# Kernel tuning notes

Measured on AMD Instinct MI355X. Metric: run time of the kernel, lower is better.

Reference implementation:

```python
import jax, jax.numpy as jnp
from jax import lax
import numpy as np

WS = 8        # window size
SHIFT = 4     # shift size
HEADS = 4
EPS = 1e-5


def _rel_pos_index(ws):
    coords = np.stack(np.meshgrid(np.arange(ws), np.arange(ws), indexing='ij'))  # (2,ws,ws)
    cf = coords.reshape(2, -1)
    rel = cf[:, :, None] - cf[:, None, :]           # (2,n,n)
    rel = rel.transpose(1, 2, 0).astype(np.int64)   # (n,n,2)
    rel[:, :, 0] += ws - 1
    rel[:, :, 1] += ws - 1
    rel[:, :, 0] *= 2 * ws - 1
    return rel.sum(-1)                              # (n,n)


def _attn_mask(h, w, ws, ss):
    img = np.zeros((h, w), dtype=np.float32)
    cnt = 0
    for hs in (slice(0, -ws), slice(-ws, -ss), slice(-ss, None)):
        for wsl in (slice(0, -ws), slice(-ws, -ss), slice(-ss, None)):
            img[hs, wsl] = cnt
            cnt += 1
    mw = img.reshape(h // ws, ws, w // ws, ws).transpose(0, 2, 1, 3).reshape(-1, ws * ws)
    am = mw[:, None, :] - mw[:, :, None]            # (nW,n,n)
    return np.where(am != 0, -100.0, 0.0).astype(np.float32)


def _ln(x, w, b):
    mu = x.mean(-1, keepdims=True)
    var = jnp.var(x, axis=-1, keepdims=True)
    return (x - mu) * lax.rsqrt(var + EPS) * w + b


def setup_inputs() -> dict:
    key = jax.random.key(0)
    ks = jax.random.split(key, 16)
    b, c, h, w = 4, 64, 256, 256
    hidden = 4 * c
    n_bias = (2 * WS - 1) * (2 * WS - 1)
    s = 0.02
    return {
        'x': jax.random.normal(ks[0], (b, c, h, w), jnp.float32),
        'norm1_w': jnp.ones((c,), jnp.float32),
        'norm1_b': jnp.zeros((c,), jnp.float32),
        'qkv_w': jax.random.normal(ks[1], (3 * c, c), jnp.float32) * s,
        'qkv_b': jnp.zeros((3 * c,), jnp.float32),
        'rpb': jax.random.normal(ks[2], (n_bias, HEADS), jnp.float32) * s,
        'proj_w': jax.random.normal(ks[3], (c, c), jnp.float32) * s,
        'proj_b': jnp.zeros((c,), jnp.float32),
        'norm2_w': jnp.ones((c,), jnp.float32),
        'norm2_b': jnp.zeros((c,), jnp.float32),
        'fc1_w': jax.random.normal(ks[4], (hidden, c), jnp.float32) * s,
        'fc1_b': jnp.zeros((hidden,), jnp.float32),
        'dw_w': jax.random.normal(ks[5], (hidden, 1, 5, 5), jnp.float32) * s,
        'dw_b': jnp.zeros((hidden,), jnp.float32),
        'fc2_w': jax.random.normal(ks[6], (c, hidden), jnp.float32) * s,
        'fc2_b': jnp.zeros((c,), jnp.float32),
    }


def reference(x, norm1_w, norm1_b, qkv_w, qkv_b, rpb, proj_w, proj_b,
              norm2_w, norm2_b, fc1_w, fc1_b, dw_w, dw_b, fc2_w, fc2_b):
    b, c, h, w = x.shape
    d = c // HEADS
    scale = d ** (-0.5)
    n = WS * WS

    x3 = jnp.transpose(x.reshape(b, c, h * w), (0, 2, 1))  # (b, hw, c)
    shortcut = x3
    xn = _ln(x3, norm1_w, norm1_b).reshape(b, h, w, c)

    # cyclic shift + window partition
    sx = jnp.roll(xn, (-SHIFT, -SHIFT), axis=(1, 2))
    win = sx.reshape(b, h // WS, WS, w // WS, WS, c).transpose(0, 1, 3, 2, 4, 5).reshape(-1, n, c)
    B_ = win.shape[0]

    qkv = (win @ qkv_w.T + qkv_b).reshape(B_, n, 3, HEADS, d).transpose(2, 0, 3, 1, 4)
    q, k, v = qkv[0] * scale, qkv[1], qkv[2]   # (B_, H, n, d)
    attn = jnp.einsum('bhnd,bhmd->bhnm', q, k)  # (B_, H, n, n)

    bias = rpb[jnp.asarray(_rel_pos_index(WS)).reshape(-1)].reshape(n, n, HEADS).transpose(2, 0, 1)
    attn = attn + bias[None]

    mask = jnp.asarray(_attn_mask(h, w, WS, SHIFT))  # (nW, n, n)
    nW = mask.shape[0]
    attn = attn.reshape(B_ // nW, nW, HEADS, n, n) + mask[None, :, None]
    attn = jax.nn.softmax(attn.reshape(B_, HEADS, n, n), axis=-1)

    out = jnp.einsum('bhnm,bhmd->bhnd', attn, v).transpose(0, 2, 1, 3).reshape(B_, n, c)
    out = out @ proj_w.T + proj_b

    # window reverse + un-shift
    sx = out.reshape(b, h // WS, w // WS, WS, WS, c).transpose(0, 1, 3, 2, 4, 5).reshape(b, h, w, c)
    xr = jnp.roll(sx, (SHIFT, SHIFT), axis=(1, 2)).reshape(b, h * w, c)
    x3 = shortcut + xr

    # ConvFFN
    xn = _ln(x3, norm2_w, norm2_b)
    hid = jax.nn.gelu(xn @ fc1_w.T + fc1_b, approximate=False)  # (b, hw, hidden)
    hidden = hid.shape[-1]
    himg = hid.transpose(0, 2, 1).reshape(b, hidden, h, w)
    dc = lax.conv_general_dilated(himg, dw_w, (1, 1), [(2, 2), (2, 2)],
                                  dimension_numbers=('NCHW', 'OIHW', 'NCHW'),
                                  feature_group_count=hidden)
    dc = jax.nn.gelu(dc + dw_b[None, :, None, None], approximate=False)
    hid = hid + dc.reshape(b, hidden, h * w).transpose(0, 2, 1)
    x3 = x3 + (hid @ fc2_w.T + fc2_b)

    return jnp.transpose(x3, (0, 2, 1)).reshape(b, c, h, w)
```

## Files before the change

kernel.cpp:

```cpp
#include <hip/hip_runtime.h>
#include <hip/hip_bf16.h>
#include <hip/hip_fp8.h>
#include <math.h>


typedef __bf16  bf16x8  __attribute__((ext_vector_type(8)));
typedef float   f32x4   __attribute__((ext_vector_type(4)));
typedef float   f32x2   __attribute__((ext_vector_type(2)));
typedef unsigned short ushortx8 __attribute__((ext_vector_type(8)));

__device__ __forceinline__ float gelu_f(float v) {
    float u = v * fmaf(0.0713548354f, v * v, 1.5957691216f);
    float t = __expf(u);
    float r = __builtin_amdgcn_rcpf(t + 1.0f);
    return v - v * r;
}
__device__ __forceinline__ unsigned char f32_to_fp8(float v) {
    __hip_fp8_e4m3 t(v);
    return (unsigned char)t.__x;
}
__device__ __forceinline__ float fp8_to_f32(unsigned char u) {
    __hip_fp8_e4m3 t;
    t.__x = (__hip_fp8_storage_t)u;
    return (float)t;
}

#if __has_builtin(__builtin_amdgcn_cvt_pk_f32_fp8) && __has_builtin(__builtin_amdgcn_cvt_pk_fp8_f32)
#define HW_FP8 1
#endif
template<bool HI>
__device__ __forceinline__ f32x2 fp8x2_f32(unsigned int u) {
#ifdef HW_FP8
    return __builtin_amdgcn_cvt_pk_f32_fp8((int)u, HI);
#else
    f32x2 r;
    const int s = HI ? 16 : 0;
    r.x = fp8_to_f32((unsigned char)(u >> s));
    r.y = fp8_to_f32((unsigned char)(u >> (s + 8)));
    return r;
#endif
}
template<bool HI>
__device__ __forceinline__ unsigned int f32x2_fp8(float a, float b, unsigned int old) {
#ifdef HW_FP8
    return (unsigned int)__builtin_amdgcn_cvt_pk_fp8_f32(a, b, (int)old, HI);
#else
    unsigned int v = (unsigned int)f32_to_fp8(a) | ((unsigned int)f32_to_fp8(b) << 8);
    return HI ? ((old & 0x0000ffffu) | (v << 16)) : ((old & 0xffff0000u) | v);
#endif
}

__device__ __forceinline__ unsigned short f2bf(float f) {
    unsigned int u = __builtin_bit_cast(unsigned int, f);
    u += 0x7fffu + ((u >> 16) & 1u);
    return (unsigned short)(u >> 16);
}
__device__ __forceinline__ float bf2f(unsigned short u) {
    return __builtin_bit_cast(float, ((unsigned int)u) << 16);
}

__global__ __launch_bounds__(256) void k_prep(
        const float* __restrict__ qkvw, const float* __restrict__ projw,
        const float* __restrict__ rpb,  const float* __restrict__ fc1w,
        unsigned short* __restrict__ qkvw_bf, unsigned short* __restrict__ projw_bf,
        unsigned short* __restrict__ rpb_bf,  unsigned short* __restrict__ fc1w_bf) {
    const int i = blockIdx.x * 256 + threadIdx.x;
    if (i < 12288) qkvw_bf[i] = f2bf(qkvw[i]);
    if (i < 4096)  projw_bf[i] = f2bf(projw[i]);
    if (i < 900)   rpb_bf[i]   = f2bf(rpb[i]);
    if (i < 16384) fc1w_bf[i]  = f2bf(fc1w[i]);
}

__global__ __launch_bounds__(256) void k_cvt(const float* __restrict__ src,
        unsigned short* __restrict__ dst, int n) {
    const int i = blockIdx.x * 256 + threadIdx.x;
    if (i < n) dst[i] = f2bf(src[i]);
}

__global__ __launch_bounds__(256) void k_ln1(const float* __restrict__ x,
        const float* __restrict__ w1, const float* __restrict__ b1,
        unsigned short* __restrict__ A, unsigned short* __restrict__ Bw) {
    __shared__ float tile[64 * 65];
    __shared__ float red0[256], red1[256];
    __shared__ float muv[64], rsv[64], lw[64], lb[64];
    const int tid = threadIdx.x;
    const int gid = blockIdx.x;
    const int xc = gid & 3, y = (gid >> 2) & 255, b = gid >> 10;
    const int x0 = xc * 64;
    if (tid < 64) { lw[tid] = w1[tid]; lb[tid] = b1[tid]; }

    const float* xb = x + ((size_t)b * 64) * 65536 + y * 256 + x0;
    {
        const int tk = tid & 63, cl = tid >> 6;
        for (int it = 0; it < 16; ++it) {
            int cc = cl + 4 * it;
            tile[cc * 65 + tk] = xb[(size_t)cc * 65536 + tk];
        }
    }
    __syncthreads();
    {
        const int tk = tid & 63, cl = tid >> 6;
        float s = 0.f, s2 = 0.f;
        #pragma unroll
        for (int k = 0; k < 16; ++k) {
            float v = tile[(cl * 16 + k) * 65 + tk];
            s += v; s2 += v * v;
        }
        red0[cl * 64 + tk] = s; red1[cl * 64 + tk] = s2;
    }
    __syncthreads();
    if (tid < 64) {
        float s  = red0[tid] + red0[64 + tid] + red0[128 + tid] + red0[192 + tid];
        float s2 = red1[tid] + red1[64 + tid] + red1[128 + tid] + red1[192 + tid];
        float mu = s * (1.f / 64.f);
        float var = s2 * (1.f / 64.f) - mu * mu;
        muv[tid] = mu; rsv[tid] = rsqrtf(var + 1e-5f);
    }
    __syncthreads();
    const int ch = tid & 63, tl = tid >> 6;
    const int ys = (y + 252) & 255;
    const int wy = ys >> 3, py = ys & 7;
    for (int it = 0; it < 16; ++it) {
        int t = tl + 4 * it;
        float v = tile[ch * 65 + t];
        int tok = (b << 16) + y * 256 + x0 + t;
        A[(size_t)tok * 64 + ch] = f2bf(v);
        float vn = (v - muv[t]) * rsv[t] * lw[ch] + lb[ch];
        int xs = (x0 + t + 252) & 255;
        int wx = xs >> 3, px = xs & 7;
        int widx = (b << 10) + (wy << 5) + wx;
        int pos = (py << 3) + px;
        Bw[((size_t)widx * 64 + pos) * 64 + ch] = f2bf(vn);
    }
}

__global__ __launch_bounds__(256) void k_attn(
        const unsigned short* __restrict__ Bw,
        const unsigned short* __restrict__ qkvw_bf,
        const unsigned short* __restrict__ projw_bf,
        const unsigned short* __restrict__ rpb_bf,
        const float* __restrict__ qkvb,
        const float* __restrict__ projb,
        const unsigned short* __restrict__ A, unsigned short* __restrict__ Cb) {
    __shared__ __align__(16) unsigned short Xs[4608];
    __shared__ __align__(16) unsigned short Ws[13824];
    __shared__ __align__(8)  unsigned short rpbl[900];
    __shared__ float qkvbl[192];
    __shared__ float projbl[64];

    const int tid = threadIdx.x;
    const int lane = tid & 63, wv = tid >> 6;
    const int l15 = lane & 15, quad = lane >> 4;
    const int widx = blockIdx.x;
    const int wib = widx & 1023;
    const int wy = wib >> 5, wx = wib & 31, bimg = widx >> 10;
    const bool edge = (wy == 31) | (wx == 31);

    const f32x4 zz = {0.f, 0.f, 0.f, 0.f};
    const ushortx8 zu = {0, 0, 0, 0, 0, 0, 0, 0};
    const bf16x8 z8 = __builtin_bit_cast(bf16x8, zu);

    const ushortx8 pw0 = *(const ushortx8*)(projw_bf + tid * 8);
    const ushortx8 pw1 = *(const ushortx8*)(projw_bf + (256 + tid) * 8);

    {
        const unsigned short* Xg = Bw + (size_t)widx * 4096 + wv * 1024;
        #pragma unroll
        for (int it = 0; it < 2; ++it) {
            int g = it * 64 + lane;
            int row = g >> 3, c8 = g & 7;
            *(ushortx8*)&Xs[(wv * 16 + row) * 72 + c8 * 8] =
                *(const ushortx8*)(Xg + g * 8);
        }
    }
    #pragma unroll
    for (int it = 0; it < 6; ++it) {
        int g = it * 256 + tid;
        int row = g >> 3, c8 = g & 7;
        *(ushortx8*)&Ws[row * 72 + c8 * 8] = *(const ushortx8*)(qkvw_bf + g * 8);
    }
    if (tid < 225) *(uint2*)&rpbl[tid * 4] = *(const uint2*)(rpb_bf + tid * 4);
    if (tid < 192) qkvbl[tid] = qkvb[tid];
    if (tid < 64)  projbl[tid] = projb[tid];
    __syncthreads();

    f32x4 qacc[12];
    #pragma unroll
    for (int i = 0; i < 12; ++i) qacc[i] = zz;
    {
        const bf16x8 av0 = *(const bf16x8*)&Xs[(16 * wv + l15) * 72 + quad * 8];
        const bf16x8 av1 = *(const bf16x8*)&Xs[(16 * wv + l15) * 72 + 32 + quad * 8];
        #pragma unroll
        for (int gl = 0; gl < 12; ++gl) {
            bf16x8 bv0 = *(const bf16x8*)&Ws[(gl * 16 + l15) * 72 + quad * 8];
            qacc[gl] = __builtin_amdgcn_mfma_f32_16x16x32_bf16(av0, bv0, qacc[gl], 0, 0, 0);
            bf16x8 bv1 = *(const bf16x8*)&Ws[(gl * 16 + l15) * 72 + 32 + quad * 8];
            qacc[gl] = __builtin_amdgcn_mfma_f32_16x16x32_bf16(av1, bv1, qacc[gl], 0, 0, 0);
        }
    }
    __syncthreads();

    #pragma unroll
    for (int g = 0; g < 12; ++g) {
        #pragma unroll
        for (int r = 0; r < 4; ++r) {
            int tok = 16 * wv + quad * 4 + r;
            int oc  = g * 16 + l15;
            float v = qacc[g][r] + qkvbl[oc];
            if (g < 4)       Ws[g * 1024 + tok * 16 + l15] = f2bf(v * 0.25f);
            else if (g < 8)  Ws[4096 + (g - 4) * 1024 + tok * 16 + l15] = f2bf(v);
            else             Ws[8192 + ((g - 8) * 16 + l15) * 72 + tok] = f2bf(v);
        }
    }
    __syncthreads();

    f32x4 sacc[4][4];
    #pragma unroll
    for (int h = 0; h < 4; ++h) {
        bf16x8 qa = z8;
        if (quad < 2) qa = *(const bf16x8*)&Ws[h * 1024 + (16 * wv + l15) * 16 + quad * 8];
        #pragma unroll
        for (int nt = 0; nt < 4; ++nt) {
            bf16x8 kf = z8;
            if (quad < 2) kf = *(const bf16x8*)&Ws[4096 + h * 1024 + (nt * 16 + l15) * 16 + quad * 8];
            sacc[h][nt] = __builtin_amdgcn_mfma_f32_16x16x32_bf16(qa, kf, zz, 0, 0, 0);
        }
    }
    __syncthreads();

    {
        const int r0 = tid >> 3;
        *(ushortx8*)&Ws[4096 + r0 * 64 + (((tid & 7) ^ (r0 & 7)) << 3)] = pw0;
        const int g1 = 256 + tid, r1 = g1 >> 3;
        *(ushortx8*)&Ws[4096 + r1 * 64 + (((g1 & 7) ^ (r1 & 7)) << 3)] = pw1;
    }

    const int jhi = l15 >> 3, jlo = l15 & 7;
    int offj4[4], regj[4];
    #pragma unroll
    for (int nt = 0; nt < 4; ++nt) {
        int j = nt * 16 + l15;
        int jy = j >> 3, jx = j & 7;
        offj4[nt] = (jy * 15 + jx) * 4;
        regj[nt] = 0;
        if (edge) {
            int ysj = wy * 8 + jy, xsj = wx * 8 + jx;
            regj[nt] = (ysj >= 252 ? 2 : (ysj >= 248 ? 1 : 0)) * 3
                     + (xsj >= 252 ? 2 : (xsj >= 248 ? 1 : 0));
        }
    }
    int rbA[4], regiA[4], pbaseA[4], i7A[4];
    #pragma unroll
    for (int r = 0; r < 4; ++r) {
        const int i = 16 * wv + quad * 4 + r;
        const int iy = i >> 3, ix = i & 7;
        rbA[r] = ((iy + 7) * 15 + (ix + 7)) * 4;
        i7A[r] = i & 7;
        pbaseA[r] = i * 64 + jlo;
        regiA[r] = 0;
        if (edge) {
            const int ysi = wy * 8 + iy, xsi = wx * 8 + ix;
            regiA[r] = (ysi >= 252 ? 2 : (ysi >= 248 ? 1 : 0)) * 3
                     + (xsi >= 252 ? 2 : (xsi >= 248 ? 1 : 0));
        }
    }

    f32x4 o[4];
    #pragma unroll
    for (int h = 0; h < 4; ++h) {
        float invh[4];
        #pragma unroll
        for (int r = 0; r < 4; ++r) {
            float m0 = -1e30f;
            #pragma unroll
            for (int nt = 0; nt < 4; ++nt) {
                float s = sacc[h][nt][r] + bf2f(rpbl[rbA[r] + h - offj4[nt]]);
                if (edge) s += (regj[nt] == regiA[r]) ? 0.f : -100.f;
                sacc[h][nt][r] = s;
                m0 = fmaxf(m0, s);
            }
            m0 = fmaxf(m0, __shfl_xor(m0, 1));
            m0 = fmaxf(m0, __shfl_xor(m0, 2));
            m0 = fmaxf(m0, __shfl_xor(m0, 4));
            m0 = fmaxf(m0, __shfl_xor(m0, 8));
            float s0 = 0.f;
            #pragma unroll
            for (int nt = 0; nt < 4; ++nt) {
                float e = __expf(sacc[h][nt][r] - m0);
                s0 += e;
                Ws[pbaseA[r] + ((((nt << 1) | jhi) ^ i7A[r]) << 3)] = f2bf(e);
            }
            s0 += __shfl_xor(s0, 1); s0 += __shfl_xor(s0, 2);
            s0 += __shfl_xor(s0, 4); s0 += __shfl_xor(s0, 8);
            invh[r] = 1.f / s0;
        }
        o[h] = zz;
        #pragma unroll
        for (int s = 0; s < 2; ++s) {
            bf16x8 pa = *(const bf16x8*)&Ws[(16 * wv + l15) * 64
                                            + (((s * 4 + quad) ^ (l15 & 7)) << 3)];
            bf16x8 vb = *(const bf16x8*)&Ws[8192 + (h * 16 + l15) * 72 + s * 32 + quad * 8];
            o[h] = __builtin_amdgcn_mfma_f32_16x16x32_bf16(pa, vb, o[h], 0, 0, 0);
        }
        #pragma unroll
        for (int r = 0; r < 4; ++r) o[h][r] *= invh[r];
    }

    unsigned short resid[16];
    #pragma unroll
    for (int r = 0; r < 4; ++r) {
        int tok = 16 * wv + quad * 4 + r;
        int py = tok >> 3, px = tok & 7;
        int yo = (wy * 8 + py + 4) & 255, xo = (wx * 8 + px + 4) & 255;
        size_t gt = ((size_t)bimg << 16) + yo * 256 + xo;
        #pragma unroll
        for (int nt = 0; nt < 4; ++nt)
            resid[r * 4 + nt] = A[gt * 64 + nt * 16 + l15];
    }

    #pragma unroll
    for (int h = 0; h < 4; ++h)
        #pragma unroll
        for (int r = 0; r < 4; ++r)
            Xs[(16 * wv + quad * 4 + r) * 72 + h * 16 + l15] = f2bf(o[h][r]);
    __syncthreads();

    f32x4 pacc[4];
    #pragma unroll
    for (int nt = 0; nt < 4; ++nt) {
        pacc[nt] = zz;
        #pragma unroll
        for (int s = 0; s < 2; ++s) {
            bf16x8 oa = *(const bf16x8*)&Xs[(16 * wv + l15) * 72 + s * 32 + quad * 8];
            bf16x8 wb = *(const bf16x8*)&Ws[4096 + (nt * 16 + l15) * 64
                                            + (((s * 4 + quad) ^ (l15 & 7)) << 3)];
            pacc[nt] = __builtin_amdgcn_mfma_f32_16x16x32_bf16(oa, wb, pacc[nt], 0, 0, 0);
        }
    }

    #pragma unroll
    for (int r = 0; r < 4; ++r) {
        int tok = 16 * wv + quad * 4 + r;
        int py = tok >> 3, px = tok & 7;
        int yo = (wy * 8 + py + 4) & 255, xo = (wx * 8 + px + 4) & 255;
        size_t gt = ((size_t)bimg << 16) + yo * 256 + xo;
        #pragma unroll
        for (int nt = 0; nt < 4; ++nt) {
            int oc = nt * 16 + l15;
            float v = pacc[nt][r] + projbl[oc] + bf2f(resid[r * 4 + nt]);
            Cb[gt * 64 + oc] = f2bf(v);
        }
    }
}

__global__ __launch_bounds__(256) void k_ln2fc1(const unsigned short* __restrict__ Cb,
        const float* __restrict__ w2, const float* __restrict__ b2,
        const unsigned short* __restrict__ fc1w_bf, const float* __restrict__ fc1b,
        unsigned char* __restrict__ D) {
    __shared__ __align__(16) unsigned short Xb[64 * 72];
    __shared__ __align__(16) unsigned short Wb[256 * 72];
    __shared__ float red0[256], red1[256];
    __shared__ float muv[64], rsv[64], lwv[64], lbv[64], fb[256];
    const int tid = threadIdx.x, gid = blockIdx.x;
    const int xc = gid & 3, y = (gid >> 2) & 255, b = gid >> 10;
    const int x0 = xc * 64;
    const int lane = tid & 63, wv = tid >> 6;
    const int l15 = lane & 15, quad = lane >> 4;
    const f32x4 zz = {0.f, 0.f, 0.f, 0.f};

    if (tid < 64) { lwv[tid] = w2[tid]; lbv[tid] = b2[tid]; }
    fb[tid] = fc1b[tid];

    const unsigned short* Cp = Cb + ((size_t)(b << 16) + y * 256 + x0) * 64;
    #pragma unroll
    for (int it = 0; it < 16; ++it) {
        int tt = wv + 4 * it;
        Xb[tt * 72 + lane] = Cp[tt * 64 + lane];
    }
    {
        const ushortx8* w8 = (const ushortx8*)fc1w_bf;
        #pragma unroll
        for (int it = 0; it < 8; ++it) {
            int idx = it * 256 + tid;
            int row = idx >> 3, c8 = idx & 7;
            *(ushortx8*)&Wb[row * 72 + c8 * 8] = w8[idx];
        }
    }
    __syncthreads();
    {
        const int tok = tid & 63, cl = tid >> 6;
        float s = 0.f, s2 = 0.f;
        #pragma unroll
        for (int g = 0; g < 2; ++g) {
            const ushortx8 u = *(const ushortx8*)&Xb[tok * 72 + cl * 16 + g * 8];
            #pragma unroll
            for (int k = 0; k < 8; ++k) { float v = bf2f(u[k]); s += v; s2 += v * v; }
        }
        red0[cl * 64 + tok] = s; red1[cl * 64 + tok] = s2;
    }
    __syncthreads();
    if (tid < 64) {
        float s  = red0[tid] + red0[64 + tid] + red0[128 + tid] + red0[192 + tid];
        float s2 = red1[tid] + red1[64 + tid] + red1[128 + tid] + red1[192 + tid];
        float mu = s * (1.f / 64.f);
        float var = s2 * (1.f / 64.f) - mu * mu;
        muv[tid] = mu; rsv[tid] = rsqrtf(var + 1e-5f);
    }
    __syncthreads();
    #pragma unroll
    for (int it = 0; it < 16; ++it) {
        int tt = wv + 4 * it;
        float v = bf2f(Xb[tt * 72 + lane]);
        v = (v - muv[tt]) * rsv[tt] * lwv[lane] + lbv[lane];
        Xb[tt * 72 + lane] = f2bf(v);
    }
    __syncthreads();

    f32x4 acc[4][4];
    #pragma unroll
    for (int mt = 0; mt < 4; ++mt)
        #pragma unroll
        for (int nt = 0; nt < 4; ++nt) acc[mt][nt] = zz;
    #pragma unroll
    for (int s = 0; s < 2; ++s) {
        bf16x8 Bf[4];
        #pragma unroll
        for (int nt = 0; nt < 4; ++nt)
            Bf[nt] = *(const bf16x8*)&Xb[(nt * 16 + l15) * 72 + s * 32 + quad * 8];
        #pragma unroll
        for (int mt = 0; mt < 4; ++mt) {
            bf16x8 Af = *(const bf16x8*)&Wb[(64 * wv + 16 * mt + l15) * 72 + s * 32 + quad * 8];
            #pragma unroll
            for (int nt = 0; nt < 4; ++nt)
                acc[mt][nt] = __builtin_amdgcn_mfma_f32_16x16x32_bf16(Af, Bf[nt], acc[mt][nt], 0, 0, 0);
        }
    }

    #pragma unroll
    for (int mt = 0; mt < 4; ++mt) {
        #pragma unroll
        for (int r = 0; r < 4; ++r) {
            const int mch = 64 * wv + 16 * mt + quad * 4 + r;
            const float bias = fb[mch];
            unsigned char* Dp = D + (((size_t)(b * 256 + mch)) << 16) + y * 256 + x0;
            float g0 = gelu_f(acc[mt][0][r] + bias);
            float g1 = gelu_f(acc[mt][1][r] + bias);
            float g2 = gelu_f(acc[mt][2][r] + bias);
            float g3 = gelu_f(acc[mt][3][r] + bias);
            unsigned int pk = f32x2_fp8<false>(g0, g1, 0u);
            pk = f32x2_fp8<true>(g2, g3, pk);
            Dp[l15]      = (unsigned char)(pk);
            Dp[16 + l15] = (unsigned char)(pk >> 8);
            Dp[32 + l15] = (unsigned char)(pk >> 16);
            Dp[48 + l15] = (unsigned char)(pk >> 24);
        }
    }
}

__global__ __launch_bounds__(256) void k_dwconv(const unsigned char* __restrict__ D,
        const float* __restrict__ dww, const float* __restrict__ dwb,
        unsigned char* __restrict__ E) {
    __shared__ __align__(16) float sm[20 * 68];
    const int tid = threadIdx.x, gid = blockIdx.x;
    const int xt = gid & 3, yt = (gid >> 2) & 15, pc = gid >> 6;
    const int ch = pc & 255;
    const int x0 = xt * 64, y0 = yt * 16;
    const unsigned char* Dp = D + ((size_t)pc << 16);

    for (int u = tid; u < 360; u += 256) {
        const int r = u / 18, c = u - r * 18;
        const int gy = y0 + r - 2;
        const int gxb = x0 - 4 + 4 * c;
        f32x2 lo = {0.f, 0.f}, hi = {0.f, 0.f};
        if (((unsigned)gy < 256u) && ((unsigned)gxb < 256u)) {
            const unsigned int v = *(const unsigned int*)(Dp + gy * 256 + gxb);
            lo = fp8x2_f32<false>(v);
            hi = fp8x2_f32<true>(v);
        }
        float* row = &sm[r * 68];
        if (c == 0)       *(f32x2*)&row[0]  = hi;
        else if (c == 17) *(f32x2*)&row[66] = lo;
        else { *(f32x2*)&row[4 * c - 2] = lo; *(f32x2*)&row[4 * c] = hi; }
    }
    float wr[25];
    #pragma unroll
    for (int k = 0; k < 25; ++k) wr[k] = dww[ch * 25 + k];
    const float bb = dwb[ch];
    __syncthreads();
    const int xq = tid & 15, yl = tid >> 4;
    float a0 = bb, a1 = bb, a2 = bb, a3 = bb;
    float c0 = 0.f, c1 = 0.f, c2 = 0.f, c3 = 0.f;
    #pragma unroll
    for (int ky = 0; ky < 5; ++ky) {
        const float* rowp = &sm[(yl + ky) * 68 + 4 * xq];
        float4 lo = *(const float4*)rowp;
        float4 hi = *(const float4*)(rowp + 4);
        float v[8] = {lo.x, lo.y, lo.z, lo.w, hi.x, hi.y, hi.z, hi.w};
        if (ky == 2) { c0 = v[2]; c1 = v[3]; c2 = v[4]; c3 = v[5]; }
        #pragma unroll
        for (int kx = 0; kx < 5; ++kx) {
            const float w = wr[ky * 5 + kx];
            a0 += w * v[kx];     a1 += w * v[kx + 1];
            a2 += w * v[kx + 2]; a3 += w * v[kx + 3];
        }
    }
    unsigned int pk = f32x2_fp8<false>(c0 + gelu_f(a0), c1 + gelu_f(a1), 0u);
    pk = f32x2_fp8<true>(c2 + gelu_f(a2), c3 + gelu_f(a3), pk);
    *(unsigned int*)&E[((size_t)pc << 16) + (y0 + yl) * 256 + x0 + 4 * xq] = pk;
}

__global__ __launch_bounds__(256) void k_fc2(const unsigned char* __restrict__ E,
        const unsigned short* __restrict__ Cb, const unsigned short* __restrict__ fc2w_bf,
        const float* __restrict__ fc2b, float* __restrict__ out) {
    __shared__ __align__(16) unsigned short Hb[64 * 136];
    __shared__ __align__(16) unsigned short Wb2[64 * 264];
    __shared__ __align__(16) unsigned short Cl[64 * 72];
    __shared__ float fbl[64];
    const int tid = threadIdx.x, gid = blockIdx.x;
    const int xc = gid & 3, y = (gid >> 2) & 255, b = gid >> 10;
    const int x0 = xc * 64;
    const int lane = tid & 63, wv = tid >> 6;
    const int l15 = lane & 15, quad = lane >> 4;
    const f32x4 zz = {0.f, 0.f, 0.f, 0.f};

    if (tid < 64) fbl[tid] = fc2b[tid];
    {
        const unsigned short* Cp = Cb + ((size_t)(b << 16) + y * 256 + x0) * 64;
        #pragma unroll
        for (int it = 0; it < 16; ++it) {
            int tt = wv + 4 * it;
            Cl[tt * 72 + lane] = Cp[tt * 64 + lane];
        }
    }
    {
        const ushortx8* w8 = (const ushortx8*)fc2w_bf;
        #pragma unroll
        for (int it = 0; it < 8; ++it) {
            int idx = it * 256 + tid;
            int row = idx >> 5, c8 = idx & 31;
            *(ushortx8*)&Wb2[row * 264 + c8 * 8] = w8[idx];
        }
    }

    f32x4 acc[4];
    #pragma unroll
    for (int nt = 0; nt < 4; ++nt) acc[nt] = zz;

    const int ldc = tid >> 4;
    const int tq  = tid & 15;
    unsigned int u0[8];
    #pragma unroll
    for (int it = 0; it < 8; ++it) {
        int chl = ldc + 16 * it;
        u0[it] = *(const unsigned int*)&E[(((size_t)(b * 256 + chl)) << 16) + y * 256 + x0 + 4 * tq];
    }
    __syncthreads();

    for (int kc = 0; kc < 2; ++kc) {
        #pragma unroll
        for (int it = 0; it < 8; ++it) {
            int chl = ldc + 16 * it;
            int pos = ((chl >> 3) ^ 0) ;
            f32x2 lo = fp8x2_f32<false>(u0[it]);
            f32x2 hi = fp8x2_f32<true>(u0[it]);
            float vals[4] = {lo.x, lo.y, hi.x, hi.y};
            #pragma unroll
            for (int j = 0; j < 4; ++j) {
                int tok = 4 * tq + j;
                int p = (((chl >> 3) ^ (tok >> 2)) << 3) + (chl & 7);
                Hb[tok * 136 + p] = f2bf(vals[j]);
            }
            (void)pos;
        }
        if (kc == 0) {
            #pragma unroll
            for (int it = 0; it < 8; ++it) {
                int chl = ldc + 16 * it + 128;
                u0[it] = *(const unsigned int*)&E[(((size_t)(b * 256 + chl)) << 16) + y * 256 + x0 + 4 * tq];
            }
        }
        __syncthreads();
        #pragma unroll
        for (int k32 = 0; k32 < 4; ++k32) {
            bf16x8 Af = *(const bf16x8*)&Wb2[(16 * wv + l15) * 264 + kc * 128 + k32 * 32 + quad * 8];
            const int g = k32 * 4 + quad;
            #pragma unroll
            for (int nt = 0; nt < 4; ++nt) {
                const int tok = nt * 16 + l15;
                bf16x8 Bf = *(const bf16x8*)&Hb[tok * 136 + ((g ^ (tok >> 2)) << 3)];
                acc[nt] = __builtin_amdgcn_mfma_f32_16x16x32_bf16(Af, Bf, acc[nt], 0, 0, 0);
            }
        }
        if (kc == 0) __syncthreads();
    }

    #pragma unroll
    for (int r = 0; r < 4; ++r) {
        const int oc = 16 * wv + quad * 4 + r;
        const float bias = fbl[oc];
        float* op = out + (((size_t)(b * 64 + oc)) << 16) + y * 256 + x0;
        #pragma unroll
        for (int nt = 0; nt < 4; ++nt) {
            const int tok = nt * 16 + l15;
            op[tok] = acc[nt][r] + bias + bf2f(Cl[tok * 72 + oc]);
        }
    }
}

extern "C" void kernel_launch(void* const* d_in, const int* in_sizes, int n_in,
                              void* d_out, int out_size, void* d_ws, size_t ws_size,
                              hipStream_t stream) {
    const float* x     = (const float*)d_in[0];
    const float* n1w   = (const float*)d_in[1];
    const float* n1b   = (const float*)d_in[2];
    const float* qkvw  = (const float*)d_in[3];
    const float* qkvb  = (const float*)d_in[4];
    const float* rpb   = (const float*)d_in[5];
    const float* projw = (const float*)d_in[6];
    const float* projb = (const float*)d_in[7];
    const float* n2w   = (const float*)d_in[8];
    const float* n2b   = (const float*)d_in[9];
    const float* fc1w  = (const float*)d_in[10];
    const float* fc1b  = (const float*)d_in[11];
    const float* dww   = (const float*)d_in[12];
    const float* dwb   = (const float*)d_in[13];
    const float* fc2w  = (const float*)d_in[14];
    const float* fc2b  = (const float*)d_in[15];
    float* out = (float*)d_out;

    char* ws = (char*)d_ws;
    const size_t MB = 1048576;
    unsigned short* Cbuf = (unsigned short*)ws;
    unsigned short* Ab   = (unsigned short*)(ws + 32 * MB);
    unsigned short* Bwp  = (unsigned short*)(ws + 64 * MB);
    unsigned char*  Dh   = (unsigned char*)(ws + 32 * MB);
    unsigned char*  Eh   = (unsigned char*)(ws + 96 * MB);

    unsigned short* qkvw_bf = (unsigned short*)(ws + 96 * MB);
    unsigned short* projw_bf = (unsigned short*)(ws + 96 * MB + 24576);
    unsigned short* rpb_bf   = (unsigned short*)(ws + 96 * MB + 32768);
    unsigned short* fc1w_bf  = (unsigned short*)(ws + 96 * MB + 34816);
    unsigned short* fc2w_bf  = (unsigned short*)(ws + 32 * MB);

    k_prep  <<<64,    256, 0, stream>>>(qkvw, projw, rpb, fc1w,
                                        qkvw_bf, projw_bf, rpb_bf, fc1w_bf);
    k_ln1   <<<4096,  256, 0, stream>>>(x, n1w, n1b, Ab, Bwp);
    k_attn  <<<4096,  256, 0, stream>>>(Bwp, qkvw_bf, projw_bf, rpb_bf,
                                        qkvb, projb, Ab, Cbuf);
    k_ln2fc1<<<4096,  256, 0, stream>>>(Cbuf, n2w, n2b, fc1w_bf, fc1b, Dh);
    k_dwconv<<<65536, 256, 0, stream>>>(Dh, dww, dwb, Eh);
    k_cvt   <<<64,    256, 0, stream>>>(fc2w, fc2w_bf, 16384);
    k_fc2   <<<4096,  256, 0, stream>>>(Eh, Cbuf, fc2w_bf, fc2b, out);
}
```

Before: 427.0 us.

## Retile depthwise conv to full-width rows with two output rows per thread

The depthwise 5x5 conv kernel now assigns each block a full 256-pixel-wide strip of 8 rows instead of a 64x16 tile. This removes horizontal halo loads and the branchy edge handling, since the side padding is zero-filled once. Each thread computes two vertically adjacent output rows, reusing the 6 shared-memory rows it loads across both, and the grid is halved. Vertical halo overhead rises (12 rows loaded for 8 output rows), and a launch-bounds occupancy hint is added.

```diff
diff --git a/kernel.cpp b/kernel.cpp
--- a/kernel.cpp
+++ b/kernel.cpp
@@ -457,56 +457,78 @@
     }
 }
 
-__global__ __launch_bounds__(256) void k_dwconv(const unsigned char* __restrict__ D,
+__global__ __launch_bounds__(256, 4) void k_dwconv(const unsigned char* __restrict__ D,
         const float* __restrict__ dww, const float* __restrict__ dwb,
         unsigned char* __restrict__ E) {
-    __shared__ __align__(16) float sm[20 * 68];
+    __shared__ __align__(16) float sm[12 * 264];
     const int tid = threadIdx.x, gid = blockIdx.x;
-    const int xt = gid & 3, yt = (gid >> 2) & 15, pc = gid >> 6;
+    const int yt = gid & 31, pc = gid >> 5;
     const int ch = pc & 255;
-    const int x0 = xt * 64, y0 = yt * 16;
+    const int y0 = yt * 8;
     const unsigned char* Dp = D + ((size_t)pc << 16);
 
-    for (int u = tid; u < 360; u += 256) {
-        const int r = u / 18, c = u - r * 18;
+    if (tid < 24) {
+        const int r = tid >> 1, side = tid & 1;
+        const f32x4 z4 = {0.f, 0.f, 0.f, 0.f};
+        *(f32x4*)&sm[r * 264 + side * 260] = z4;
+    }
+    #pragma unroll
+    for (int it = 0; it < 3; ++it) {
+        const int u = it * 256 + tid;
+        const int r = u >> 6, ci = u & 63;
         const int gy = y0 + r - 2;
-        const int gxb = x0 - 4 + 4 * c;
-        f32x2 lo = {0.f, 0.f}, hi = {0.f, 0.f};
-        if (((unsigned)gy < 256u) && ((unsigned)gxb < 256u)) {
-            const unsigned int v = *(const unsigned int*)(Dp + gy * 256 + gxb);
-            lo = fp8x2_f32<false>(v);
-            hi = fp8x2_f32<true>(v);
-        }
-        float* row = &sm[r * 68];
-        if (c == 0)       *(f32x2*)&row[0]  = hi;
-        else if (c == 17) *(f32x2*)&row[66] = lo;
-        else { *(f32x2*)&row[4 * c - 2] = lo; *(f32x2*)&row[4 * c] = hi; }
+        f32x4 vv = {0.f, 0.f, 0.f, 0.f};
+        if ((unsigned)gy < 256u) {
+            const unsigned int v = *(const unsigned int*)(Dp + gy * 256 + 4 * ci);
+            const f32x2 lo = fp8x2_f32<false>(v);
+            const f32x2 hi = fp8x2_f32<true>(v);
+            vv.x = lo.x; vv.y = lo.y; vv.z = hi.x; vv.w = hi.y;
+        }
+        *(f32x4*)&sm[r * 264 + 4 + 4 * ci] = vv;
     }
     float wr[25];
     #pragma unroll
     for (int k = 0; k < 25; ++k) wr[k] = dww[ch * 25 + k];
     const float bb = dwb[ch];
     __syncthreads();
-    const int xq = tid & 15, yl = tid >> 4;
-    float a0 = bb, a1 = bb, a2 = bb, a3 = bb;
-    float c0 = 0.f, c1 = 0.f, c2 = 0.f, c3 = 0.f;
-    #pragma unroll
-    for (int ky = 0; ky < 5; ++ky) {
-        const float* rowp = &sm[(yl + ky) * 68 + 4 * xq];
-        float4 lo = *(const float4*)rowp;
-        float4 hi = *(const float4*)(rowp + 4);
-        float v[8] = {lo.x, lo.y, lo.z, lo.w, hi.x, hi.y, hi.z, hi.w};
-        if (ky == 2) { c0 = v[2]; c1 = v[3]; c2 = v[4]; c3 = v[5]; }
-        #pragma unroll
-        for (int kx = 0; kx < 5; ++kx) {
-            const float w = wr[ky * 5 + kx];
-            a0 += w * v[kx];     a1 += w * v[kx + 1];
-            a2 += w * v[kx + 2]; a3 += w * v[kx + 3];
-        }
-    }
-    unsigned int pk = f32x2_fp8<false>(c0 + gelu_f(a0), c1 + gelu_f(a1), 0u);
-    pk = f32x2_fp8<true>(c2 + gelu_f(a2), c3 + gelu_f(a3), pk);
-    *(unsigned int*)&E[((size_t)pc << 16) + (y0 + yl) * 256 + x0 + 4 * xq] = pk;
+
+    const int xq = tid & 63, yl = tid >> 6;
+    float aA0 = bb, aA1 = bb, aA2 = bb, aA3 = bb;
+    float aB0 = bb, aB1 = bb, aB2 = bb, aB3 = bb;
+    float cA0, cA1, cA2, cA3, cB0, cB1, cB2, cB3;
+    #pragma unroll
+    for (int r6 = 0; r6 < 6; ++r6) {
+        const float* rowp = &sm[(2 * yl + r6) * 264 + 4 * xq + 2];
+        f32x2  p0 = *(const f32x2*)rowp;
+        float4 p1 = *(const float4*)(rowp + 2);
+        f32x2  p2 = *(const f32x2*)(rowp + 6);
+        float v[8] = {p0.x, p0.y, p1.x, p1.y, p1.z, p1.w, p2.x, p2.y};
+        if (r6 == 2) { cA0 = v[2]; cA1 = v[3]; cA2 = v[4]; cA3 = v[5]; }
+        if (r6 == 3) { cB0 = v[2]; cB1 = v[3]; cB2 = v[4]; cB3 = v[5]; }
+        if (r6 < 5) {
+            #pragma unroll
+            for (int kx = 0; kx < 5; ++kx) {
+                const float w = wr[r6 * 5 + kx];
+                aA0 += w * v[kx];     aA1 += w * v[kx + 1];
+                aA2 += w * v[kx + 2]; aA3 += w * v[kx + 3];
+            }
+        }
+        if (r6 >= 1) {
+            #pragma unroll
+            for (int kx = 0; kx < 5; ++kx) {
+                const float w = wr[(r6 - 1) * 5 + kx];
+                aB0 += w * v[kx];     aB1 += w * v[kx + 1];
+                aB2 += w * v[kx + 2]; aB3 += w * v[kx + 3];
+            }
+        }
+    }
+    unsigned int pkA = f32x2_fp8<false>(cA0 + gelu_f(aA0), cA1 + gelu_f(aA1), 0u);
+    pkA = f32x2_fp8<true>(cA2 + gelu_f(aA2), cA3 + gelu_f(aA3), pkA);
+    unsigned int pkB = f32x2_fp8<false>(cB0 + gelu_f(aB0), cB1 + gelu_f(aB1), 0u);
+    pkB = f32x2_fp8<true>(cB2 + gelu_f(aB2), cB3 + gelu_f(aB3), pkB);
+    unsigned char* Ep = E + ((size_t)pc << 16) + (y0 + 2 * yl) * 256 + 4 * xq;
+    *(unsigned int*)Ep         = pkA;
+    *(unsigned int*)(Ep + 256) = pkB;
 }
 
 __global__ __launch_bounds__(256) void k_fc2(const unsigned char* __restrict__ E,
@@ -560,7 +582,6 @@
         #pragma unroll
         for (int it = 0; it < 8; ++it) {
             int chl = ldc + 16 * it;
-            int pos = ((chl >> 3) ^ 0) ;
             f32x2 lo = fp8x2_f32<false>(u0[it]);
             f32x2 hi = fp8x2_f32<true>(u0[it]);
             float vals[4] = {lo.x, lo.y, hi.x, hi.y};
@@ -570,7 +591,6 @@
                 int p = (((chl >> 3) ^ (tok >> 2)) << 3) + (chl & 7);
                 Hb[tok * 136 + p] = f2bf(vals[j]);
             }
-            (void)pos;
         }
         if (kc == 0) {
             #pragma unroll
@@ -648,7 +668,7 @@
     k_attn  <<<4096,  256, 0, stream>>>(Bwp, qkvw_bf, projw_bf, rpb_bf,
                                         qkvb, projb, Ab, Cbuf);
     k_ln2fc1<<<4096,  256, 0, stream>>>(Cbuf, n2w, n2b, fc1w_bf, fc1b, Dh);
-    k_dwconv<<<65536, 256, 0, stream>>>(Dh, dww, dwb, Eh);
+    k_dwconv<<<32768, 256, 0, stream>>>(Dh, dww, dwb, Eh);
     k_cvt   <<<64,    256, 0, stream>>>(fc2w, fc2w_bf, 16384);
     k_fc2   <<<4096,  256, 0, stream>>>(Eh, Cbuf, fc2w_bf, fc2b, out);
 }
```

Result: faster. 413.5 us (-3.2%).

## Recast depthwise 5x5 conv as banded-Toeplitz MFMA matmuls with larger tiles

Applied to the files above, without the earlier changes.

The depthwise conv kernel now computes each output row segment as a bf16 MFMA. The 5-tap horizontal filter for each kernel row is expanded into a banded Toeplitz A matrix held in shared memory, and the input rows are converted from fp8 to bf16 into a padded shared tile. Blocks now cover 32 full-width rows instead of 16x64 tiles, which cuts the grid from 65536 to 8192 blocks and the halo reloads. Outputs are staged through shared memory so global stores are 16-byte. The band matrix wastes most of the MFMA multiplies, and the weights and center value are now rounded to bf16, which slightly changes precision.

```diff
diff --git a/kernel.cpp b/kernel.cpp
--- a/kernel.cpp
+++ b/kernel.cpp
@@ -460,53 +460,85 @@
 __global__ __launch_bounds__(256) void k_dwconv(const unsigned char* __restrict__ D,
         const float* __restrict__ dww, const float* __restrict__ dwb,
         unsigned char* __restrict__ E) {
-    __shared__ __align__(16) float sm[20 * 68];
+    __shared__ __align__(16) unsigned short inT[36 * 280 + 16];
+    __shared__ __align__(16) unsigned short Atab[5 * 64 * 8];
+    __shared__ __align__(16) unsigned char outT[4][16 * 144];
     const int tid = threadIdx.x, gid = blockIdx.x;
-    const int xt = gid & 3, yt = (gid >> 2) & 15, pc = gid >> 6;
+    const int yt = gid & 7, pc = gid >> 3;
     const int ch = pc & 255;
-    const int x0 = xt * 64, y0 = yt * 16;
+    const int y0 = yt * 32;
     const unsigned char* Dp = D + ((size_t)pc << 16);
-
-    for (int u = tid; u < 360; u += 256) {
-        const int r = u / 18, c = u - r * 18;
-        const int gy = y0 + r - 2;
-        const int gxb = x0 - 4 + 4 * c;
-        f32x2 lo = {0.f, 0.f}, hi = {0.f, 0.f};
-        if (((unsigned)gy < 256u) && ((unsigned)gxb < 256u)) {
-            const unsigned int v = *(const unsigned int*)(Dp + gy * 256 + gxb);
-            lo = fp8x2_f32<false>(v);
-            hi = fp8x2_f32<true>(v);
-        }
-        float* row = &sm[r * 68];
-        if (c == 0)       *(f32x2*)&row[0]  = hi;
-        else if (c == 17) *(f32x2*)&row[66] = lo;
-        else { *(f32x2*)&row[4 * c - 2] = lo; *(f32x2*)&row[4 * c] = hi; }
-    }
-    float wr[25];
-    #pragma unroll
-    for (int k = 0; k < 25; ++k) wr[k] = dww[ch * 25 + k];
+    const f32x4 zz = {0.f, 0.f, 0.f, 0.f};
+
+    #pragma unroll
+    for (int it = 0; it < 5; ++it) {
+        int idx = it * 256 + tid;
+        if (idx < 1262) ((uint4*)inT)[idx] = make_uint4(0, 0, 0, 0);
+    }
+    __syncthreads();
+
+    #pragma unroll
+    for (int it = 0; it < 9; ++it) {
+        const int u = it * 256 + tid;
+        const int t = u >> 6, c = u & 63;
+        const int gy = y0 - 2 + t;
+        if ((unsigned)gy < 256u) {
+            const unsigned int v = *(const unsigned int*)(Dp + gy * 256 + 4 * c);
+            const f32x2 lo = fp8x2_f32<false>(v);
+            const f32x2 hi = fp8x2_f32<true>(v);
+            unsigned int b01 = (unsigned)f2bf(lo.x) | ((unsigned)f2bf(lo.y) << 16);
+            unsigned int b23 = (unsigned)f2bf(hi.x) | ((unsigned)f2bf(hi.y) << 16);
+            unsigned int* base = (unsigned int*)&inT[t * 280 + 2 + 4 * c];
+            base[0] = b01; base[1] = b23;
+        }
+    }
+    #pragma unroll
+    for (int q = 0; q < 10; ++q) {
+        const int e = tid * 10 + q;
+        const int ky = e >> 9, r = e & 511;
+        const int l = r >> 3, j = r & 7;
+        const int m = l & 15, k = ((l >> 4) << 3) + j;
+        const int d = k - m;
+        float wv = 0.f;
+        if (d >= 0 && d < 5) wv = dww[ch * 25 + ky * 5 + d];
+        Atab[e] = f2bf(wv);
+    }
     const float bb = dwb[ch];
     __syncthreads();
-    const int xq = tid & 15, yl = tid >> 4;
-    float a0 = bb, a1 = bb, a2 = bb, a3 = bb;
-    float c0 = 0.f, c1 = 0.f, c2 = 0.f, c3 = 0.f;
-    #pragma unroll
-    for (int ky = 0; ky < 5; ++ky) {
-        const float* rowp = &sm[(yl + ky) * 68 + 4 * xq];
-        float4 lo = *(const float4*)rowp;
-        float4 hi = *(const float4*)(rowp + 4);
-        float v[8] = {lo.x, lo.y, lo.z, lo.w, hi.x, hi.y, hi.z, hi.w};
-        if (ky == 2) { c0 = v[2]; c1 = v[3]; c2 = v[4]; c3 = v[5]; }
-        #pragma unroll
-        for (int kx = 0; kx < 5; ++kx) {
-            const float w = wr[ky * 5 + kx];
-            a0 += w * v[kx];     a1 += w * v[kx + 1];
-            a2 += w * v[kx + 2]; a3 += w * v[kx + 3];
-        }
-    }
-    unsigned int pk = f32x2_fp8<false>(c0 + gelu_f(a0), c1 + gelu_f(a1), 0u);
-    pk = f32x2_fp8<true>(c2 + gelu_f(a2), c3 + gelu_f(a3), pk);
-    *(unsigned int*)&E[((size_t)pc << 16) + (y0 + yl) * 256 + x0 + 4 * xq] = pk;
+
+    const int wv_ = tid >> 6, lane = tid & 63;
+    const int l15 = lane & 15, quad = lane >> 4;
+    const int g = wv_ >> 1, xh = wv_ & 1;
+    bf16x8 Af[5];
+    #pragma unroll
+    for (int ky = 0; ky < 5; ++ky)
+        Af[ky] = *(const bf16x8*)&Atab[(ky * 64 + lane) * 8];
+    const int tbase = g * 16 + l15;
+
+    #pragma unroll
+    for (int xp = 0; xp < 8; ++xp) {
+        const int xs = xh * 128 + xp * 16;
+        f32x4 acc = zz;
+        #pragma unroll
+        for (int ky = 0; ky < 5; ++ky) {
+            bf16x8 Bf = *(const bf16x8*)&inT[(tbase + ky) * 280 + xs + quad * 8];
+            acc = __builtin_amdgcn_mfma_f32_16x16x32_bf16(Af[ky], Bf, acc, 0, 0, 0);
+        }
+        const unsigned int* cp32 = (const unsigned int*)&inT[(tbase + 2) * 280 + 2 + xs + quad * 4];
+        const unsigned int c01 = cp32[0], c23 = cp32[1];
+        const float c0 = bf2f((unsigned short)c01), c1 = bf2f((unsigned short)(c01 >> 16));
+        const float c2 = bf2f((unsigned short)c23), c3 = bf2f((unsigned short)(c23 >> 16));
+        unsigned int pk = f32x2_fp8<false>(c0 + gelu_f(acc[0] + bb), c1 + gelu_f(acc[1] + bb), 0u);
+        pk = f32x2_fp8<true>(c2 + gelu_f(acc[2] + bb), c3 + gelu_f(acc[3] + bb), pk);
+        *(unsigned int*)&outT[wv_][l15 * 144 + xp * 16 + quad * 4] = pk;
+    }
+
+    {
+        const int row = lane >> 2, sg = lane & 3;
+        unsigned char* Ep = E + ((size_t)pc << 16) + (y0 + g * 16 + row) * 256 + xh * 128 + sg * 32;
+        *(uint4*)Ep        = *(const uint4*)&outT[wv_][row * 144 + sg * 32];
+        *(uint4*)(Ep + 16) = *(const uint4*)&outT[wv_][row * 144 + sg * 32 + 16];
+    }
 }
 
 __global__ __launch_bounds__(256) void k_fc2(const unsigned char* __restrict__ E,
@@ -560,7 +592,6 @@
         #pragma unroll
         for (int it = 0; it < 8; ++it) {
             int chl = ldc + 16 * it;
-            int pos = ((chl >> 3) ^ 0) ;
             f32x2 lo = fp8x2_f32<false>(u0[it]);
             f32x2 hi = fp8x2_f32<true>(u0[it]);
             float vals[4] = {lo.x, lo.y, hi.x, hi.y};
@@ -570,7 +601,6 @@
                 int p = (((chl >> 3) ^ (tok >> 2)) << 3) + (chl & 7);
                 Hb[tok * 136 + p] = f2bf(vals[j]);
             }
-            (void)pos;
         }
         if (kc == 0) {
             #pragma unroll
@@ -648,7 +678,7 @@
     k_attn  <<<4096,  256, 0, stream>>>(Bwp, qkvw_bf, projw_bf, rpb_bf,
                                         qkvb, projb, Ab, Cbuf);
     k_ln2fc1<<<4096,  256, 0, stream>>>(Cbuf, n2w, n2b, fc1w_bf, fc1b, Dh);
-    k_dwconv<<<65536, 256, 0, stream>>>(Dh, dww, dwb, Eh);
+    k_dwconv<<<8192,  256, 0, stream>>>(Dh, dww, dwb, Eh);
     k_cvt   <<<64,    256, 0, stream>>>(fc2w, fc2w_bf, 16384);
     k_fc2   <<<4096,  256, 0, stream>>>(Eh, Cbuf, fc2w_bf, fc2b, out);
 }
```

Result: faster. 389.4 us (-8.8%).
